# Kernel tuning notes

Measured on AMD Instinct MI355X. Metric: run time of the kernel, lower is better.

The kernel has to match this reference:

```python
import jax, jax.numpy as jnp
import numpy as np

LN_EPS = 1e-5
SCALE = 1.0 / 8.0  # 1/sqrt(dim/num_heads) = 1/sqrt(64)


def layernorm(x, g, b):
    m = jnp.mean(x, axis=-1, keepdims=True)
    v = jnp.mean(jnp.square(x - m), axis=-1, keepdims=True)
    return (x - m) * jax.lax.rsqrt(v + LN_EPS) * g + b


def attention_block(q_in, kv_in, wq, bq, wk, bk, wv, bv, g, b):
    # un-split single-matrix attention, faithful to the source (no head reshape)
    Q = q_in @ wq + bq            # [B,S,D]
    K = kv_in @ wk + bk           # [B,T,D]
    V = kv_in @ wv + bv           # [B,T,D]
    scores = jnp.einsum('bsd,btd->bst', Q, K) * SCALE  # [B,S,T]
    A = jax.nn.softmax(scores, axis=-1)
    out = jnp.einsum('bst,btd->bsd', A, V)
    return layernorm(out + q_in, g, b)


def setup_inputs() -> dict:
    key = jax.random.key(0)
    ks = jax.random.split(key, 16)
    B, S, T, D = 4, 2048, 2048, 1024
    w = lambda k: jax.random.normal(k, (D, D), dtype=jnp.float32) * 0.02
    z = jnp.zeros((D,), dtype=jnp.float32)
    o = jnp.ones((D,), dtype=jnp.float32)
    return {
        'x': jax.random.normal(ks[0], (B, S, D), dtype=jnp.float32),
        'y': jax.random.normal(ks[1], (B, T, D), dtype=jnp.float32),
        'wq_m': w(ks[2]), 'bq_m': z, 'wk_m': w(ks[3]), 'bk_m': z,
        'wv_m': w(ks[4]), 'bv_m': z, 'g_m': o, 'b_m': z,
        'wq_c': w(ks[5]), 'bq_c': z, 'wk_c': w(ks[6]), 'bk_c': z,
        'wv_c': w(ks[7]), 'bv_c': z, 'g_c': o, 'b_c': z,
        'f0_w': w(ks[8]), 'f0_b': z, 'f1_w': w(ks[9]), 'f1_b': z,
        'g_d': o, 'b_d': z,
    }


def reference(x, y,
              wq_m, bq_m, wk_m, bk_m, wv_m, bv_m, g_m, b_m,
              wq_c, bq_c, wk_c, bk_c, wv_c, bv_c, g_c, b_c,
              f0_w, f0_b, f1_w, f1_b, g_d, b_d):
    # masked (self) attention + shared decoder LN residual
    res = x
    x = layernorm(attention_block(x, x, wq_m, bq_m, wk_m, bk_m, wv_m, bv_m, g_m, b_m) + res, g_d, b_d)
    # cross attention against memory y
    res = x
    x = layernorm(attention_block(x, y, wq_c, bq_c, wk_c, bk_c, wv_c, bv_c, g_c, b_c) + res, g_d, b_d)
    # FFN: loop condition in source is always true -> GELU (exact) after every layer
    res = x
    x = jax.nn.gelu(x @ f0_w + f0_b, approximate=False)
    x = jax.nn.gelu(x @ f1_w + f1_b, approximate=False)
    return layernorm(x + res, g_d, b_d)
```

## Files before the change

### kernel.cpp

```cpp
#include <hip/hip_runtime.h>

#define DEV __device__ __forceinline__

typedef __attribute__((ext_vector_type(8))) short bf16x8;
typedef __attribute__((ext_vector_type(4))) float f32x4;

DEV float bf2f(unsigned short u) { return __uint_as_float(((unsigned int)u) << 16); }
DEV unsigned short f2bf(float f) {
    unsigned int x = __float_as_uint(f);
    return (unsigned short)((x + 0x7fffu + ((x >> 16) & 1u)) >> 16);
}
DEV float gelu_exact(float x) { return 0.5f * x * (1.0f + erff(x * 0.7071067811865475f)); }

DEV void gload16(const void* g, void* l) {
    __builtin_amdgcn_global_load_lds((const __attribute__((address_space(1))) void*)g,
                                     (__attribute__((address_space(3))) void*)l, 16, 0, 0);
}

template <int OFF>
DEV bf16x8 ds_read128(unsigned addr) {
    bf16x8 r;
    asm volatile("ds_read_b128 %0, %1 offset:%2" : "=v"(r) : "v"(addr), "i"(OFF));
    return r;
}

__global__ __launch_bounds__(256) void transpose_cast_w(const float* __restrict__ in,
                                                        unsigned short* __restrict__ out,
                                                        int R, int C) {
    __shared__ float tile[32][33];
    int c0 = blockIdx.x * 32, r0 = blockIdx.y * 32;
    int tx = threadIdx.x, ty = threadIdx.y;
#pragma unroll
    for (int i = 0; i < 32; i += 8)
        tile[ty + i][tx] = in[(size_t)(r0 + ty + i) * C + (c0 + tx)];
    __syncthreads();
#pragma unroll
    for (int i = 0; i < 32; i += 8)
        out[(size_t)(c0 + ty + i) * R + (r0 + tx)] = f2bf(tile[tx][ty + i]);
}

__global__ __launch_bounds__(256) void cast_f32_bf16(const float* __restrict__ in,
                                                     unsigned short* __restrict__ out, int n4) {
    int i = blockIdx.x * 256 + threadIdx.x;
    if (i >= n4) return;
    float4 v = ((const float4*)in)[i];
    unsigned short o[4] = {f2bf(v.x), f2bf(v.y), f2bf(v.z), f2bf(v.w)};
    *(uint2*)(out + (size_t)i * 4) = *(uint2*)o;
}


template <int Q>
DEV void mfma16(const bf16x8 (&a)[2][2], const bf16x8 (&b)[4][2], f32x4 (&acc)[8][4]) {
#pragma unroll
    for (int ks = 0; ks < 2; ++ks)
#pragma unroll
        for (int n = 0; n < 4; ++n) {
            acc[2 * Q][n]     = __builtin_amdgcn_mfma_f32_16x16x32_bf16(a[0][ks], b[n][ks], acc[2 * Q][n], 0, 0, 0);
            acc[2 * Q + 1][n] = __builtin_amdgcn_mfma_f32_16x16x32_bf16(a[1][ks], b[n][ks], acc[2 * Q + 1][n], 0, 0, 0);
        }
}

template <int BIAS_MODE, bool GELU_ACT, bool OUT_F32>
__global__ __launch_bounds__(512, 2) void gemm256(const unsigned short* __restrict__ A,
                                                  const unsigned short* __restrict__ BT,
                                                  const float* __restrict__ bias,
                                                  float* __restrict__ Cf,
                                                  unsigned short* __restrict__ Cb,
                                                  int N, int K, int lda, int ldb, float scale,
                                                  long sA, long sB, long sC, long sBias) {
    A += (long)blockIdx.z * sA;
    BT += (long)blockIdx.z * sB;
    if (BIAS_MODE) bias += (long)blockIdx.z * sBias;

    const int tid = threadIdx.x;
    const int lane = tid & 63;
    const int wave = tid >> 6;
    const int wm = wave >> 2;
    const int wn = wave & 3;
    const int llo = lane & 15, lhi = lane >> 4;
    const int bm = blockIdx.x * 256, bn = blockIdx.y * 256;
    const int brow = (wn & 1) * 64;

    __shared__ unsigned short lds[2][4][128 * 64];

    const int xk0 = (0 + lhi) ^ (llo & 7);
    const int xk1 = (4 + lhi) ^ (llo & 7);

    const unsigned ldsA = (unsigned)(size_t)&lds[0][wm][0] + (unsigned)llo * 128u;
    const unsigned ldsB = (unsigned)(size_t)&lds[0][2 + (wn >> 1)][0] + (unsigned)(brow + llo) * 128u;
    unsigned aA[2][2], aB[2][2];
    aA[0][0] = ldsA + xk0 * 16; aA[0][1] = ldsA + xk1 * 16;
    aA[1][0] = aA[0][0] + 65536u; aA[1][1] = aA[0][1] + 65536u;
    aB[0][0] = ldsB + xk0 * 16; aB[0][1] = ldsB + xk1 * 16;
    aB[1][0] = aB[0][0] + 65536u; aB[1][1] = aB[0][1] + 65536u;

    const int d0 = wave * 64 + lane;
    const int sr0 = d0 >> 3, sq0 = (d0 & 7) ^ (sr0 & 7);
    const int d1 = 512 + d0;
    const int sr1 = d1 >> 3, sq1 = (d1 & 7) ^ (sr1 & 7);

    const unsigned short* gA0 = A + (size_t)bm * lda;
    const unsigned short* gA1 = A + (size_t)(bm + 128) * lda;
    const unsigned short* gB0 = BT + (size_t)bn * ldb;
    const unsigned short* gB1 = BT + (size_t)(bn + 128) * ldb;

#define STAGE(grow, ld, kt, l)                                                          \
    {                                                                                   \
        gload16((grow) + (size_t)sr0 * (ld) + (kt) + sq0 * 8, (l) + wave * 512);        \
        gload16((grow) + (size_t)sr1 * (ld) + (kt) + sq1 * 8, (l) + 4096 + wave * 512); \
    }

    f32x4 acc[8][4] = {};
    bf16x8 b[4][2];

#define PH(Q, BUF, LOADB, STG, TAIL)                                         \
    {                                                                        \
        bf16x8 afr[2][2];                                                    \
        afr[0][0] = ds_read128<(Q)*4096>(aA[BUF][0]);                        \
        afr[0][1] = ds_read128<(Q)*4096>(aA[BUF][1]);                        \
        afr[1][0] = ds_read128<(Q)*4096 + 2048>(aA[BUF][0]);                 \
        afr[1][1] = ds_read128<(Q)*4096 + 2048>(aA[BUF][1]);                 \
        if (LOADB) {                                                         \
            b[0][0] = ds_read128<0>(aB[BUF][0]);                             \
            b[0][1] = ds_read128<0>(aB[BUF][1]);                             \
            b[1][0] = ds_read128<2048>(aB[BUF][0]);                          \
            b[1][1] = ds_read128<2048>(aB[BUF][1]);                          \
            b[2][0] = ds_read128<4096>(aB[BUF][0]);                          \
            b[2][1] = ds_read128<4096>(aB[BUF][1]);                          \
            b[3][0] = ds_read128<6144>(aB[BUF][0]);                          \
            b[3][1] = ds_read128<6144>(aB[BUF][1]);                          \
        }                                                                    \
        STG;                                                                 \
        __builtin_amdgcn_s_barrier();                                        \
        asm volatile("s_waitcnt lgkmcnt(0)" :::);                            \
        __builtin_amdgcn_sched_barrier(0); \
        __builtin_amdgcn_s_setprio(1);                                       \
        mfma16<Q>(afr, b, acc);                                              \
        __builtin_amdgcn_s_setprio(0);                                       \
        TAIL;                                                                \
        __builtin_amdgcn_s_barrier();                                        \
    }

#define VM4 asm volatile("s_waitcnt vmcnt(4)" :::)
#define VM0 asm volatile("s_waitcnt vmcnt(0)" :::)
#define NOP ((void)0)

    const int nt = K >> 6;
    const int niter = nt >> 1;

    STAGE(gA0, lda, 0, lds[0][0]);
    STAGE(gA1, lda, 0, lds[0][1]);
    STAGE(gB0, ldb, 0, lds[0][2]);
    STAGE(gB1, ldb, 0, lds[0][3]);
    STAGE(gB0, ldb, 64, lds[1][2]);
    STAGE(gB1, ldb, 64, lds[1][3]);
    VM4;
    __builtin_amdgcn_s_barrier();

    int kt = 0;
    for (int i = 0; i < niter - 1; ++i) {
        const int kt1 = kt + 64, kt2 = kt + 128, kt3 = kt + 192;
        PH(0, 0, true,  STAGE(gA0, lda, kt1, lds[1][0]), NOP);
        PH(1, 0, false, STAGE(gA1, lda, kt1, lds[1][1]), NOP);
        PH(2, 0, false, STAGE(gB0, ldb, kt2, lds[0][2]), NOP);
        PH(3, 0, false, STAGE(gB1, ldb, kt2, lds[0][3]), VM4);
        PH(0, 1, true,  STAGE(gA0, lda, kt2, lds[0][0]), NOP);
        PH(1, 1, false, STAGE(gA1, lda, kt2, lds[0][1]), NOP);
        PH(2, 1, false, STAGE(gB0, ldb, kt3, lds[1][2]), NOP);
        PH(3, 1, false, STAGE(gB1, ldb, kt3, lds[1][3]), VM4);
        kt += 128;
    }
    {
        const int kt1 = kt + 64;
        PH(0, 0, true,  STAGE(gA0, lda, kt1, lds[1][0]), NOP);
        PH(1, 0, false, STAGE(gA1, lda, kt1, lds[1][1]), NOP);
        PH(2, 0, false, NOP, NOP);
        PH(3, 0, false, NOP, VM0);
        PH(0, 1, true,  NOP, NOP);
        PH(1, 1, false, NOP, NOP);
        PH(2, 1, false, NOP, NOP);
        PH(3, 1, false, NOP, NOP);
    }
#undef PH
#undef STAGE
#undef VM4
#undef VM0
#undef NOP

#pragma unroll
    for (int m = 0; m < 8; ++m) {
#pragma unroll
        for (int n = 0; n < 4; ++n) {
            const int col = bn + wn * 64 + n * 16 + llo;
            float bcol = 0.f;
            if constexpr (BIAS_MODE == 1) bcol = bias[col];
#pragma unroll
            for (int j = 0; j < 4; ++j) {
                const int row = bm + wm * 128 + m * 16 + lhi * 4 + j;
                float v = acc[m][n][j] * scale + bcol;
                if constexpr (BIAS_MODE == 2) v += bias[row];
                if constexpr (GELU_ACT) v = gelu_exact(v);
                const size_t idx = (size_t)blockIdx.z * (size_t)sC + (size_t)row * N + col;
                if constexpr (OUT_F32) Cf[idx] = v;
                else Cb[idx] = f2bf(v);
            }
        }
    }
}

__global__ __launch_bounds__(256) void softmax_rows(unsigned short* __restrict__ s, int T) {
    __shared__ float red[4];
    unsigned short* p = s + (size_t)blockIdx.x * T;
    const int tid = threadIdx.x;

    uint4 raw = *(const uint4*)(p + tid * 8);
    const unsigned short* u = (const unsigned short*)&raw;
    float v[8];
#pragma unroll
    for (int j = 0; j < 8; ++j) v[j] = bf2f(u[j]);

    float mx = -3.4e38f;
#pragma unroll
    for (int j = 0; j < 8; ++j) mx = fmaxf(mx, v[j]);
#pragma unroll
    for (int o = 32; o; o >>= 1) mx = fmaxf(mx, __shfl_xor(mx, o));
    if ((tid & 63) == 0) red[tid >> 6] = mx;
    __syncthreads();
    mx = fmaxf(fmaxf(red[0], red[1]), fmaxf(red[2], red[3]));
    __syncthreads();

    float sum = 0.f;
#pragma unroll
    for (int j = 0; j < 8; ++j) {
        v[j] = expf(v[j] - mx);
        sum += v[j];
    }
#pragma unroll
    for (int o = 32; o; o >>= 1) sum += __shfl_xor(sum, o);
    if ((tid & 63) == 0) red[tid >> 6] = sum;
    __syncthreads();
    sum = red[0] + red[1] + red[2] + red[3];
    const float inv = 1.0f / sum;

    unsigned short o8[8];
#pragma unroll
    for (int j = 0; j < 8; ++j) o8[j] = f2bf(v[j] * inv);
    *(uint4*)(p + tid * 8) = *(uint4*)o8;
}

DEV float block_sum(float v, float* red, int tid) {
#pragma unroll
    for (int o = 32; o; o >>= 1) v += __shfl_xor(v, o);
    if ((tid & 63) == 0) red[tid >> 6] = v;
    __syncthreads();
    v = red[0] + red[1] + red[2] + red[3];
    __syncthreads();
    return v;
}

__global__ __launch_bounds__(256) void ln_double(const float* __restrict__ av,
                                                 const float* __restrict__ xin,
                                                 const float* __restrict__ g1, const float* __restrict__ b1,
                                                 const float* __restrict__ g2, const float* __restrict__ b2,
                                                 float* __restrict__ xout,
                                                 unsigned short* __restrict__ xbf, int D) {
    __shared__ float red[4];
    const int tid = threadIdx.x;
    const size_t base = (size_t)blockIdx.x * D + tid * 4;
    const float4 a4 = *(const float4*)(av + base);
    const float4 x4 = *(const float4*)(xin + base);
    float x[4] = {x4.x, x4.y, x4.z, x4.w};
    float t[4] = {a4.x + x[0], a4.y + x[1], a4.z + x[2], a4.w + x[3]};
    const float invD = 1.0f / D;

    float m = block_sum(t[0] + t[1] + t[2] + t[3], red, tid) * invD;
    float q = 0.f;
#pragma unroll
    for (int j = 0; j < 4; ++j) q += (t[j] - m) * (t[j] - m);
    q = block_sum(q, red, tid) * invD;
    float rs = rsqrtf(q + 1e-5f);

    float u[4];
#pragma unroll
    for (int j = 0; j < 4; ++j) {
        const int idx = tid * 4 + j;
        u[j] = (t[j] - m) * rs * g1[idx] + b1[idx] + x[j];
    }
    float m2 = block_sum(u[0] + u[1] + u[2] + u[3], red, tid) * invD;
    float q2 = 0.f;
#pragma unroll
    for (int j = 0; j < 4; ++j) q2 += (u[j] - m2) * (u[j] - m2);
    q2 = block_sum(q2, red, tid) * invD;
    float rs2 = rsqrtf(q2 + 1e-5f);

    float4 o4;
    unsigned short ob[4];
#pragma unroll
    for (int j = 0; j < 4; ++j) {
        const int idx = tid * 4 + j;
        float o = (u[j] - m2) * rs2 * g2[idx] + b2[idx];
        ((float*)&o4)[j] = o;
        ob[j] = f2bf(o);
    }
    *(float4*)(xout + base) = o4;
    *(uint2*)(xbf + base) = *(uint2*)ob;
}

__global__ __launch_bounds__(256) void ln_single(const float* __restrict__ a,
                                                 const float* __restrict__ b_,
                                                 const float* __restrict__ g, const float* __restrict__ bb,
                                                 float* __restrict__ out, int D) {
    __shared__ float red[4];
    const int tid = threadIdx.x;
    const size_t base = (size_t)blockIdx.x * D + tid * 4;
    const float4 a4 = *(const float4*)(a + base);
    const float4 x4 = *(const float4*)(b_ + base);
    float t[4] = {a4.x + x4.x, a4.y + x4.y, a4.z + x4.z, a4.w + x4.w};
    const float invD = 1.0f / D;
    float m = block_sum(t[0] + t[1] + t[2] + t[3], red, tid) * invD;
    float q = 0.f;
#pragma unroll
    for (int j = 0; j < 4; ++j) q += (t[j] - m) * (t[j] - m);
    q = block_sum(q, red, tid) * invD;
    float rs = rsqrtf(q + 1e-5f);
    float4 o4;
#pragma unroll
    for (int j = 0; j < 4; ++j) {
        const int idx = tid * 4 + j;
        ((float*)&o4)[j] = (t[j] - m) * rs * g[idx] + bb[idx];
    }
    *(float4*)(out + base) = o4;
}

extern "C" void kernel_launch(void* const* d_in, const int* in_sizes, int n_in,
                              void* d_out, int out_size, void* d_ws, size_t ws_size,
                              hipStream_t stream) {
    (void)in_sizes; (void)n_in; (void)out_size; (void)ws_size;
    constexpr int B = 4, S = 2048, T = 2048, D = 1024;
    constexpr int M = B * S;
    constexpr long MD = (long)M * D;
    constexpr long ST = (long)S * T;
    constexpr long DD = (long)D * D;

    const float* x = (const float*)d_in[0];
    const float* y = (const float*)d_in[1];
    const float* w_in[8] = {(const float*)d_in[2],  (const float*)d_in[4],  (const float*)d_in[6],
                            (const float*)d_in[10], (const float*)d_in[12], (const float*)d_in[14],
                            (const float*)d_in[18], (const float*)d_in[20]};
    const float* bq_m = (const float*)d_in[3];
    const float* bk_m = (const float*)d_in[5];
    const float* bv_m = (const float*)d_in[7];
    const float* g_m = (const float*)d_in[8];
    const float* b_m = (const float*)d_in[9];
    const float* bq_c = (const float*)d_in[11];
    const float* bk_c = (const float*)d_in[13];
    const float* bv_c = (const float*)d_in[15];
    const float* g_c = (const float*)d_in[16];
    const float* b_c = (const float*)d_in[17];
    const float* f0_b = (const float*)d_in[19];
    const float* f1_b = (const float*)d_in[21];
    const float* g_d = (const float*)d_in[22];
    const float* b_d = (const float*)d_in[23];
    float* dout = (float*)d_out;

    char* p = (char*)d_ws;
    auto carve = [&](size_t bytes) { void* r = p; p += (bytes + 255) & ~(size_t)255; return r; };
    float* xcur = (float*)carve(MD * 4);
    unsigned short* wT = (unsigned short*)carve((size_t)8 * DD * 2);
    unsigned short* abf = (unsigned short*)carve(MD * 2);
    unsigned short* ybf = (unsigned short*)carve(MD * 2);
    unsigned short* Qb = (unsigned short*)carve(MD * 2);
    unsigned short* Kb = (unsigned short*)carve(MD * 2);
    unsigned short* Vt = (unsigned short*)carve(MD * 2);
    unsigned short* scores = (unsigned short*)carve((size_t)B * ST * 2);
    float* tmp = (float*)carve(MD * 4);
    float* bqk_m = (float*)carve(2 * D * 4);
    float* bqk_c = (float*)carve(2 * D * 4);

    const dim3 blk256(256), blk512(512);
    const dim3 tb(32, 8);

    for (int w = 0; w < 8; ++w)
        transpose_cast_w<<<dim3(32, 32), tb, 0, stream>>>(w_in[w], wT + (size_t)w * DD, D, D);
    cast_f32_bf16<<<dim3(M * D / 4 / 256), blk256, 0, stream>>>(x, abf, M * D / 4);
    cast_f32_bf16<<<dim3(M * D / 4 / 256), blk256, 0, stream>>>(y, ybf, M * D / 4);
    hipMemcpyAsync(bqk_m, bq_m, D * 4, hipMemcpyDeviceToDevice, stream);
    hipMemcpyAsync(bqk_m + D, bk_m, D * 4, hipMemcpyDeviceToDevice, stream);
    hipMemcpyAsync(bqk_c, bq_c, D * 4, hipMemcpyDeviceToDevice, stream);
    hipMemcpyAsync(bqk_c + D, bk_c, D * 4, hipMemcpyDeviceToDevice, stream);

    unsigned short* wqm = wT + 0 * DD;
    unsigned short* wvm = wT + 2 * DD;
    unsigned short* wqc = wT + 3 * DD;
    unsigned short* wvc = wT + 5 * DD;
    unsigned short* wf0 = wT + 6 * DD;
    unsigned short* wf1 = wT + 7 * DD;

    const dim3 gQK(M / 256, D / 256, 2);
    const dim3 gVt(D / 256, T / 256, B);
    const dim3 gScores(S / 256, T / 256, B);
    const dim3 gPV(S / 256, D / 256, B);
    const dim3 gFFN(M / 256, D / 256, 1);

    gemm256<1, false, false><<<gQK, blk512, 0, stream>>>(abf, wqm, bqk_m, nullptr, Qb, D, D, D, D, 1.f, 0, DD, MD, D);
    gemm256<2, false, false><<<gVt, blk512, 0, stream>>>(wvm, abf, bv_m, nullptr, Vt, T, D, D, D, 1.f, 0, (long)S * D, (long)D * T, 0);
    gemm256<0, false, false><<<gScores, blk512, 0, stream>>>(Qb, Kb, nullptr, nullptr, scores, T, D, D, D, 0.125f, (long)S * D, (long)T * D, ST, 0);
    softmax_rows<<<dim3(B * S), blk256, 0, stream>>>(scores, T);
    gemm256<0, false, true><<<gPV, blk512, 0, stream>>>(scores, Vt, nullptr, tmp, nullptr, D, T, T, T, 1.f, ST, (long)T * D, (long)S * D, 0);
    ln_double<<<dim3(M), blk256, 0, stream>>>(tmp, x, g_m, b_m, g_d, b_d, xcur, abf, D);

    gemm256<1, false, false><<<gQK, blk512, 0, stream>>>(abf, wqc, bqk_c, nullptr, Qb, D, D, D, D, 1.f, MD, DD, MD, D);
    gemm256<2, false, false><<<gVt, blk512, 0, stream>>>(wvc, ybf, bv_c, nullptr, Vt, T, D, D, D, 1.f, 0, (long)S * D, (long)D * T, 0);
    gemm256<0, false, false><<<gScores, blk512, 0, stream>>>(Qb, Kb, nullptr, nullptr, scores, T, D, D, D, 0.125f, (long)S * D, (long)T * D, ST, 0);
    softmax_rows<<<dim3(B * S), blk256, 0, stream>>>(scores, T);
    gemm256<0, false, true><<<gPV, blk512, 0, stream>>>(scores, Vt, nullptr, tmp, nullptr, D, T, T, T, 1.f, ST, (long)T * D, (long)S * D, 0);
    ln_double<<<dim3(M), blk256, 0, stream>>>(tmp, xcur, g_c, b_c, g_d, b_d, xcur, abf, D);

    gemm256<1, true, false><<<gFFN, blk512, 0, stream>>>(abf, wf0, f0_b, nullptr, Qb, D, D, D, D, 1.f, 0, 0, 0, 0);
    gemm256<1, true, true><<<gFFN, blk512, 0, stream>>>(Qb, wf1, f1_b, tmp, nullptr, D, D, D, D, 1.f, 0, 0, 0, 0);
    ln_single<<<dim3(M), blk256, 0, stream>>>(tmp, xcur, g_d, b_d, dout, D);
}
```

Before: 549.2 us.

## Merge GEMM phases into two-phase schedule and remap workgroups across XCDs

Restructures the 256x256 bf16 GEMM main loop from four phases per k-tile to two, each issuing 32 MFMAs over four A fragments, with the global-to-LDS staging moved ahead of the LDS reads. This halves the number of barrier pairs per k-tile, at the cost of more A-fragment registers held live. It also adds a workgroup index remap that interleaves blocks across the 8 XCDs so neighbouring tiles share L2. The remap assumes the total block count is divisible by 8; otherwise some tiles are computed twice and others never.

```diff
diff --git a/kernel.cpp b/kernel.cpp
--- a/kernel.cpp
+++ b/kernel.cpp
@@ -49,15 +49,16 @@
 }
 
 
-template <int Q>
-DEV void mfma16(const bf16x8 (&a)[2][2], const bf16x8 (&b)[4][2], f32x4 (&acc)[8][4]) {
+template <int H>
+DEV void mfma32(const bf16x8 (&a)[4][2], const bf16x8 (&b)[4][2], f32x4 (&acc)[8][4]) {
 #pragma unroll
     for (int ks = 0; ks < 2; ++ks)
 #pragma unroll
-        for (int n = 0; n < 4; ++n) {
-            acc[2 * Q][n]     = __builtin_amdgcn_mfma_f32_16x16x32_bf16(a[0][ks], b[n][ks], acc[2 * Q][n], 0, 0, 0);
-            acc[2 * Q + 1][n] = __builtin_amdgcn_mfma_f32_16x16x32_bf16(a[1][ks], b[n][ks], acc[2 * Q + 1][n], 0, 0, 0);
-        }
+        for (int mi = 0; mi < 4; ++mi)
+#pragma unroll
+            for (int n = 0; n < 4; ++n)
+                acc[4 * H + mi][n] =
+                    __builtin_amdgcn_mfma_f32_16x16x32_bf16(a[mi][ks], b[n][ks], acc[4 * H + mi][n], 0, 0, 0);
 }
 
 template <int BIAS_MODE, bool GELU_ACT, bool OUT_F32>
@@ -68,9 +69,18 @@
                                                   unsigned short* __restrict__ Cb,
                                                   int N, int K, int lda, int ldb, float scale,
                                                   long sA, long sB, long sC, long sBias) {
-    A += (long)blockIdx.z * sA;
-    BT += (long)blockIdx.z * sB;
-    if (BIAS_MODE) bias += (long)blockIdx.z * sBias;
+    const int gx = gridDim.x, gy = gridDim.y;
+    int f = blockIdx.x + gx * (blockIdx.y + gy * blockIdx.z);
+    const int nwg = gx * gy * gridDim.z;
+    f = (f & 7) * (nwg >> 3) + (f >> 3);
+    const int bz = f / (gx * gy);
+    const int rem = f - bz * gx * gy;
+    const int by = rem / gx;
+    const int bx = rem - by * gx;
+
+    A += (long)bz * sA;
+    BT += (long)bz * sB;
+    if (BIAS_MODE) bias += (long)bz * sBias;
 
     const int tid = threadIdx.x;
     const int lane = tid & 63;
@@ -78,7 +88,7 @@
     const int wm = wave >> 2;
     const int wn = wave & 3;
     const int llo = lane & 15, lhi = lane >> 4;
-    const int bm = blockIdx.x * 256, bn = blockIdx.y * 256;
+    const int bm = bx * 256, bn = by * 256;
     const int brow = (wn & 1) * 64;
 
     __shared__ unsigned short lds[2][4][128 * 64];
@@ -109,17 +119,24 @@
         gload16((grow) + (size_t)sr0 * (ld) + (kt) + sq0 * 8, (l) + wave * 512);        \
         gload16((grow) + (size_t)sr1 * (ld) + (kt) + sq1 * 8, (l) + 4096 + wave * 512); \
     }
+#define SA(kt, BUF) { STAGE(gA0, lda, kt, lds[BUF][0]); STAGE(gA1, lda, kt, lds[BUF][1]); }
+#define SB(kt, BUF) { STAGE(gB0, ldb, kt, lds[BUF][2]); STAGE(gB1, ldb, kt, lds[BUF][3]); }
 
     f32x4 acc[8][4] = {};
     bf16x8 b[4][2];
 
-#define PH(Q, BUF, LOADB, STG, TAIL)                                         \
+#define PH2(H, BUF, LOADB, STG, TAIL)                                        \
     {                                                                        \
-        bf16x8 afr[2][2];                                                    \
-        afr[0][0] = ds_read128<(Q)*4096>(aA[BUF][0]);                        \
-        afr[0][1] = ds_read128<(Q)*4096>(aA[BUF][1]);                        \
-        afr[1][0] = ds_read128<(Q)*4096 + 2048>(aA[BUF][0]);                 \
-        afr[1][1] = ds_read128<(Q)*4096 + 2048>(aA[BUF][1]);                 \
+        STG;                                                                 \
+        bf16x8 afr[4][2];                                                    \
+        afr[0][0] = ds_read128<(H)*8192 + 0>(aA[BUF][0]);                    \
+        afr[0][1] = ds_read128<(H)*8192 + 0>(aA[BUF][1]);                    \
+        afr[1][0] = ds_read128<(H)*8192 + 2048>(aA[BUF][0]);                 \
+        afr[1][1] = ds_read128<(H)*8192 + 2048>(aA[BUF][1]);                 \
+        afr[2][0] = ds_read128<(H)*8192 + 4096>(aA[BUF][0]);                 \
+        afr[2][1] = ds_read128<(H)*8192 + 4096>(aA[BUF][1]);                 \
+        afr[3][0] = ds_read128<(H)*8192 + 6144>(aA[BUF][0]);                 \
+        afr[3][1] = ds_read128<(H)*8192 + 6144>(aA[BUF][1]);                 \
         if (LOADB) {                                                         \
             b[0][0] = ds_read128<0>(aB[BUF][0]);                             \
             b[0][1] = ds_read128<0>(aB[BUF][1]);                             \
@@ -130,12 +147,11 @@
             b[3][0] = ds_read128<6144>(aB[BUF][0]);                          \
             b[3][1] = ds_read128<6144>(aB[BUF][1]);                          \
         }                                                                    \
-        STG;                                                                 \
         __builtin_amdgcn_s_barrier();                                        \
         asm volatile("s_waitcnt lgkmcnt(0)" :::);                            \
-        __builtin_amdgcn_sched_barrier(0); \
+        __builtin_amdgcn_sched_barrier(0);                                   \
         __builtin_amdgcn_s_setprio(1);                                       \
-        mfma16<Q>(afr, b, acc);                                              \
+        mfma32<H>(afr, b, acc);                                              \
         __builtin_amdgcn_s_setprio(0);                                       \
         TAIL;                                                                \
         __builtin_amdgcn_s_barrier();                                        \
@@ -148,40 +164,31 @@
     const int nt = K >> 6;
     const int niter = nt >> 1;
 
-    STAGE(gA0, lda, 0, lds[0][0]);
-    STAGE(gA1, lda, 0, lds[0][1]);
-    STAGE(gB0, ldb, 0, lds[0][2]);
-    STAGE(gB1, ldb, 0, lds[0][3]);
-    STAGE(gB0, ldb, 64, lds[1][2]);
-    STAGE(gB1, ldb, 64, lds[1][3]);
+    SA(0, 0);
+    SB(0, 0);
+    SB(64, 1);
     VM4;
     __builtin_amdgcn_s_barrier();
 
     int kt = 0;
     for (int i = 0; i < niter - 1; ++i) {
         const int kt1 = kt + 64, kt2 = kt + 128, kt3 = kt + 192;
-        PH(0, 0, true,  STAGE(gA0, lda, kt1, lds[1][0]), NOP);
-        PH(1, 0, false, STAGE(gA1, lda, kt1, lds[1][1]), NOP);
-        PH(2, 0, false, STAGE(gB0, ldb, kt2, lds[0][2]), NOP);
-        PH(3, 0, false, STAGE(gB1, ldb, kt2, lds[0][3]), VM4);
-        PH(0, 1, true,  STAGE(gA0, lda, kt2, lds[0][0]), NOP);
-        PH(1, 1, false, STAGE(gA1, lda, kt2, lds[0][1]), NOP);
-        PH(2, 1, false, STAGE(gB0, ldb, kt3, lds[1][2]), NOP);
-        PH(3, 1, false, STAGE(gB1, ldb, kt3, lds[1][3]), VM4);
+        PH2(0, 0, true,  SA(kt1, 1), NOP);
+        PH2(1, 0, false, SB(kt2, 0), VM4);
+        PH2(0, 1, true,  SA(kt2, 0), NOP);
+        PH2(1, 1, false, SB(kt3, 1), VM4);
         kt += 128;
     }
     {
         const int kt1 = kt + 64;
-        PH(0, 0, true,  STAGE(gA0, lda, kt1, lds[1][0]), NOP);
-        PH(1, 0, false, STAGE(gA1, lda, kt1, lds[1][1]), NOP);
-        PH(2, 0, false, NOP, NOP);
-        PH(3, 0, false, NOP, VM0);
-        PH(0, 1, true,  NOP, NOP);
-        PH(1, 1, false, NOP, NOP);
-        PH(2, 1, false, NOP, NOP);
-        PH(3, 1, false, NOP, NOP);
-    }
-#undef PH
+        PH2(0, 0, true,  SA(kt1, 1), NOP);
+        PH2(1, 0, false, NOP, VM0);
+        PH2(0, 1, true,  NOP, NOP);
+        PH2(1, 1, false, NOP, NOP);
+    }
+#undef PH2
+#undef SA
+#undef SB
 #undef STAGE
 #undef VM4
 #undef VM0
@@ -200,7 +207,7 @@
                 float v = acc[m][n][j] * scale + bcol;
                 if constexpr (BIAS_MODE == 2) v += bias[row];
                 if constexpr (GELU_ACT) v = gelu_exact(v);
-                const size_t idx = (size_t)blockIdx.z * (size_t)sC + (size_t)row * N + col;
+                const size_t idx = (size_t)bz * (size_t)sC + (size_t)row * N + col;
                 if constexpr (OUT_F32) Cf[idx] = v;
                 else Cb[idx] = f2bf(v);
             }
```

Result: slower. 576.3 us (+4.9%).
